# Kernel optimization log

Hardware: AMD Instinct MI355X
Metric: run time of the kernel (lower is better)

## Reference

```python
import jax, jax.numpy as jnp
import numpy as np

# SemiConv2d with semifield_type='MaxMin':
#   out[n,oc,i,j] = max_{ic,kh,kw} min(x_pad[n,ic,i+kh,j+kw], kernel[oc,ic,kh,kw])
# stride=1, 'same' padding with -inf (identity of max).

def setup_inputs() -> dict:
    key = jax.random.key(0)
    kx, kk = jax.random.split(key)
    x = jax.random.normal(kx, (8, 32, 96, 96), dtype=jnp.float32)
    kernel = jax.random.normal(kk, (32, 32, 3, 3), dtype=jnp.float32)
    return {"x": x, "kernel": kernel}


def reference(x, kernel):
    N, IC, H, W = x.shape
    OC, IC2, KH, KW = kernel.shape
    assert IC == IC2
    # same padding for k=3, stride=1 (left=top=1, right=bottom=1)
    p = KH - 1
    top = left = p // 2
    bot = right = p - top
    xp = jnp.pad(x, ((0, 0), (0, 0), (top, bot), (left, right)),
                 constant_values=-jnp.inf)
    out = None
    # small fixed loop over kernel taps (KH*KW = 9); vectorized over N, OC, IC, H, W
    for kh in range(KH):
        for kw in range(KW):
            win = xp[:, :, kh:kh + H, kw:kw + W]           # [N, IC, H, W]
            k_tap = kernel[:, :, kh, kw]                   # [OC, IC]
            # min over values, max over input channels -> [N, OC, H, W]
            v = jnp.max(jnp.minimum(win[:, None], k_tap[None, :, :, None, None]), axis=2)
            out = v if out is None else jnp.maximum(out, v)
    return out
```

## Files before the change

kernel.cpp:

```cpp
#include <hip/hip_runtime.h>
#include <math.h>
#include <stdint.h>


#define HH 96
#define WW 96
#define CIN 32
#define OCN 32
#define XQ_ROWS 98
#define XQ_W 48
#define XQ_SLICE (XQ_ROWS * XQ_W)
#define XQ_TOTAL (256 * XQ_SLICE)
#define NROW 96
#define TBL_BYTES ((size_t)32 * NROW * 16)
#define RMX_BYTES ((size_t)32 * NROW * 4)
#define WS_NEED ((size_t)XQ_TOTAL * 8 + TBL_BYTES + RMX_BYTES)
#define NEGH2 0xFC00FC00u

typedef _Float16 h2 __attribute__((ext_vector_type(2)));
typedef uint32_t u2a4 __attribute__((ext_vector_type(2), aligned(4)));

__device__ __forceinline__ uint32_t pkmin_vs(uint32_t x, uint32_t k) {
    uint32_t d;
    asm("v_pk_min_f16 %0, %1, %2" : "=v"(d) : "v"(x), "s"(k));
    return d;
}
__device__ __forceinline__ uint32_t pkmin_vv(uint32_t a, uint32_t b) {
    uint32_t d;
    asm("v_pk_min_f16 %0, %1, %2" : "=v"(d) : "v"(a), "v"(b));
    return d;
}
__device__ __forceinline__ uint32_t pkmax(uint32_t a, uint32_t b) {
    uint32_t d;
    asm("v_pk_max_f16 %0, %1, %2" : "=v"(d) : "v"(a), "v"(b));
    return d;
}
__device__ __forceinline__ uint32_t packh2(float lo, float hi) {
    h2 p = {(_Float16)lo, (_Float16)hi};
    return __builtin_bit_cast(uint32_t, p);
}

__global__ __launch_bounds__(256) void setup_xq(const float* __restrict__ x,
                                                uint2* __restrict__ xq) {
    int idx = blockIdx.x * 256 + threadIdx.x;
    int j  = idx % XQ_W;
    int t  = idx / XQ_W;
    int hp = t % XQ_ROWS;
    int s  = t / XQ_ROWS;
    int h  = hp - 1;
    bool hv = (h >= 0) && (h < HH);
    const float* row = x + ((size_t)s * HH + (hv ? h : 0)) * WW;
    float a = (hv && j > 0)        ? row[2 * j - 1] : -INFINITY;
    float b = hv                   ? row[2 * j]     : -INFINITY;
    float c = hv                   ? row[2 * j + 1] : -INFINITY;
    float d = (hv && j < XQ_W - 1) ? row[2 * j + 2] : -INFINITY;
    uint2 v;
    v.x = packh2(a, b);
    v.y = packh2(c, d);
    xq[idx] = v;
}

__global__ void setup_row(const float* __restrict__ kk, uint4* __restrict__ tbl,
                          uint32_t* __restrict__ rmx) {
    __shared__ float rs[NROW];
    const int oc = blockIdx.x;
    const int t  = threadIdx.x;
    const int ic = t / 3, dh = t - ic * 3;
    const float* kp = kk + ((size_t)(oc * CIN + ic) * 3 + dh) * 3;
    float k0 = kp[0], k1 = kp[1], k2 = kp[2];
    float rm = fmaxf(fmaxf(k0, k1), k2);
    rs[t] = rm;
    __syncthreads();
    int rank = 0;
    for (int s = 0; s < NROW; ++s) {
        float v = rs[s];
        rank += (v > rm) || (v == rm && s < t);
    }
    uint32_t off = (uint32_t)(ic * XQ_ROWS + dh) * (XQ_W * 8);
    tbl[oc * NROW + rank] = make_uint4(packh2(k0, k0), packh2(k1, k1),
                                       packh2(k2, k2), off);
    rmx[oc * NROW + rank] = packh2(rm, rm);
}

__global__ __launch_bounds__(192, 8) void semiconv_row(const char* __restrict__ xqb,
                                                       const uint4* __restrict__ tbl,
                                                       const uint32_t* __restrict__ rmx,
                                                       float* __restrict__ out) {
    const int tid = threadIdx.x;
    const int jj = tid % 48;
    const int hr = tid / 48;
    const int b  = blockIdx.x;
    const int hp = b % 24;
    const int t  = b / 24;
    const int oc = t & 31;
    const int n  = t >> 5;
    const int h  = hp * 4 + hr;

    const char* xb = xqb + (size_t)n * CIN * XQ_SLICE * 8
                         + (size_t)(h * XQ_W + jj) * 8;
    const uint4* tb = tbl + oc * NROW;
    const uint32_t* rb = rmx + oc * NROW;

    uint32_t acc = NEGH2;
    uint4 e0 = tb[0], e1 = tb[1];

    for (int c = 0; c < NROW / 2; ++c) {
        uint4 f0, f1; uint32_t fr;
        if (c < NROW / 2 - 1) {
            const uint4* nb = tb + 2 * c + 2;
            f0 = nb[0]; f1 = nb[1];
            fr = rb[2 * c + 2];
        }
        u2a4 q0 = *(const u2a4*)(xb + e0.w);
        u2a4 q1 = *(const u2a4*)(xb + e1.w);
        uint32_t v01 = __builtin_amdgcn_alignbit(q0.y, q0.x, 16);
        uint32_t v11 = __builtin_amdgcn_alignbit(q1.y, q1.x, 16);
        uint32_t m0 = pkmax(pkmin_vs(q0.x, e0.x), pkmin_vs(v01, e0.y));
        m0 = pkmax(m0, pkmin_vs(q0.y, e0.z));
        uint32_t m1 = pkmax(pkmin_vs(q1.x, e1.x), pkmin_vs(v11, e1.y));
        m1 = pkmax(m1, pkmin_vs(q1.y, e1.z));
        acc = pkmax(acc, pkmax(m0, m1));

        if (c < NROW / 2 - 1) {
            uint32_t sw = __builtin_amdgcn_alignbit(acc, acc, 16);
            uint32_t mn = pkmin_vv(acc, sw);
            h2 a  = __builtin_bit_cast(h2, mn);
            h2 kn = __builtin_bit_cast(h2, fr);
            if (__all((float)a.x >= (float)kn.x)) break;
            e0 = f0; e1 = f1;
        }
    }

    h2 a = __builtin_bit_cast(h2, acc);
    float2 v = make_float2((float)a.x, (float)a.y);
    *(float2*)(out + (((size_t)(n * OCN + oc)) * HH + h) * WW + 2 * jj) = v;
}

#define NEGINF (-INFINITY)
__global__ __launch_bounds__(192, 8) void semiconv2d_f32(
    const float* __restrict__ x, const float* __restrict__ kk, float* __restrict__ out)
{
    const int tid = threadIdx.x;
    const int w  = tid % WW;
    const int hr = tid / WW;
    const int b   = blockIdx.x;
    const int ocb = b & 7;
    const int hp  = (b >> 3) % 48;
    const int n   = (b >> 3) / 48;
    const int h   = hp * 2 + hr;
    const int oc0 = ocb * 4;
    float a0[4], a1[4], a2[4];
#pragma unroll
    for (int i = 0; i < 4; ++i) { a0[i] = NEGINF; a1[i] = NEGINF; a2[i] = NEGINF; }
    const bool vm = (h > 0), vp = (h < HH - 1);
    const int hm  = vm ? h - 1 : h;
    const int hpl = vp ? h + 1 : h;
    const int cm  = (w > 0) ? -1 : 0;
    const int cp  = (w < WW - 1) ? 1 : 0;
    const float* rm = x + ((size_t)(n * CIN) * HH + hm)  * WW + w;
    const float* r1 = x + ((size_t)(n * CIN) * HH + h)   * WW + w;
    const float* rp = x + ((size_t)(n * CIN) * HH + hpl) * WW + w;
#pragma unroll 2
    for (int ic = 0; ic < CIN; ++ic) {
        float r00 = vm ? rm[cm] : NEGINF, r01 = vm ? rm[0] : NEGINF, r02 = vm ? rm[cp] : NEGINF;
        float r10 = r1[cm], r11 = r1[0], r12 = r1[cp];
        float r20 = vp ? rp[cm] : NEGINF, r21 = vp ? rp[0] : NEGINF, r22 = vp ? rp[cp] : NEGINF;
#pragma unroll
        for (int oc = 0; oc < 4; ++oc) {
            const float* kq = kk + (size_t)(((oc0 + oc) * CIN + ic)) * 9;
            a0[oc] = fmaxf(fmaxf(a0[oc], fminf(r00, kq[0])), fmaxf(fminf(r10, kq[3]), fminf(r20, kq[6])));
            a1[oc] = fmaxf(fmaxf(a1[oc], fminf(r01, kq[1])), fmaxf(fminf(r11, kq[4]), fminf(r21, kq[7])));
            a2[oc] = fmaxf(fmaxf(a2[oc], fminf(r02, kq[2])), fmaxf(fminf(r12, kq[5]), fminf(r22, kq[8])));
        }
        rm += HH * WW; r1 += HH * WW; rp += HH * WW;
    }
#pragma unroll
    for (int oc = 0; oc < 4; ++oc) {
        float v0 = (w > 0)      ? a0[oc] : NEGINF;
        float v2 = (w < WW - 1) ? a2[oc] : NEGINF;
        out[(((size_t)(n * OCN + oc0 + oc)) * HH + h) * WW + w] = fmaxf(fmaxf(v0, a1[oc]), v2);
    }
}

extern "C" void kernel_launch(void* const* d_in, const int* in_sizes, int n_in,
                              void* d_out, int out_size, void* d_ws, size_t ws_size,
                              hipStream_t stream) {
    const float* x  = (const float*)d_in[0];
    const float* kk = (const float*)d_in[1];
    float* out      = (float*)d_out;
    if (ws_size >= WS_NEED) {
        uint2*    xq  = (uint2*)d_ws;
        uint4*    tbl = (uint4*)((char*)d_ws + (size_t)XQ_TOTAL * 8);
        uint32_t* rmx = (uint32_t*)((char*)d_ws + (size_t)XQ_TOTAL * 8 + TBL_BYTES);
        setup_xq<<<dim3(XQ_TOTAL / 256), dim3(256), 0, stream>>>(x, xq);
        setup_row<<<dim3(32), dim3(NROW), 0, stream>>>(kk, tbl, rmx);
        semiconv_row<<<dim3(8 * 32 * 24), dim3(192), 0, stream>>>(
            (const char*)xq, tbl, rmx, out);
    } else {
        semiconv2d_f32<<<dim3(8 * 48 * 8), dim3(192), 0, stream>>>(x, kk, out);
    }
}
```

Measured before the change: 98.71 us.

## Compute four output channels per thread with grouped sorted tap table

The main kernel now has each thread compute four output channels from one load of the packed fp16 input. It walks a per-group table sorted by the group-wide maximum kernel row value, which amortizes input loads and table-entry reads across channels. The two setup kernels are merged into one launch to save a launch. The trade-off is that early exit now needs all four channels to saturate against a looser group bound, so more rows may be processed. Register pressure also rises from holding eight uint4 table entries.

```diff
diff --git a/kernel.cpp b/kernel.cpp
--- a/kernel.cpp
+++ b/kernel.cpp
@@ -11,10 +11,11 @@
 #define XQ_W 48
 #define XQ_SLICE (XQ_ROWS * XQ_W)
 #define XQ_TOTAL (256 * XQ_SLICE)
+#define XQB (XQ_TOTAL / 256)
 #define NROW 96
-#define TBL_BYTES ((size_t)32 * NROW * 16)
-#define RMX_BYTES ((size_t)32 * NROW * 4)
-#define WS_NEED ((size_t)XQ_TOTAL * 8 + TBL_BYTES + RMX_BYTES)
+#define NOCG 8
+#define TBLG_BYTES ((size_t)NOCG * NROW * 64)
+#define WS_NEED ((size_t)XQ_TOTAL * 8 + TBLG_BYTES)
 #define NEGH2 0xFC00FC00u
 
 typedef _Float16 h2 __attribute__((ext_vector_type(2)));
@@ -40,100 +41,138 @@
     return __builtin_bit_cast(uint32_t, p);
 }
 
-__global__ __launch_bounds__(256) void setup_xq(const float* __restrict__ x,
-                                                uint2* __restrict__ xq) {
-    int idx = blockIdx.x * 256 + threadIdx.x;
-    int j  = idx % XQ_W;
-    int t  = idx / XQ_W;
-    int hp = t % XQ_ROWS;
-    int s  = t / XQ_ROWS;
-    int h  = hp - 1;
-    bool hv = (h >= 0) && (h < HH);
-    const float* row = x + ((size_t)s * HH + (hv ? h : 0)) * WW;
-    float a = (hv && j > 0)        ? row[2 * j - 1] : -INFINITY;
-    float b = hv                   ? row[2 * j]     : -INFINITY;
-    float c = hv                   ? row[2 * j + 1] : -INFINITY;
-    float d = (hv && j < XQ_W - 1) ? row[2 * j + 2] : -INFINITY;
-    uint2 v;
-    v.x = packh2(a, b);
-    v.y = packh2(c, d);
-    xq[idx] = v;
-}
-
-__global__ void setup_row(const float* __restrict__ kk, uint4* __restrict__ tbl,
-                          uint32_t* __restrict__ rmx) {
+__global__ __launch_bounds__(256) void setup_all(const float* __restrict__ x,
+                                                 const float* __restrict__ kk,
+                                                 uint2* __restrict__ xq,
+                                                 uint4* __restrict__ tblg) {
     __shared__ float rs[NROW];
-    const int oc = blockIdx.x;
-    const int t  = threadIdx.x;
-    const int ic = t / 3, dh = t - ic * 3;
-    const float* kp = kk + ((size_t)(oc * CIN + ic) * 3 + dh) * 3;
-    float k0 = kp[0], k1 = kp[1], k2 = kp[2];
-    float rm = fmaxf(fmaxf(k0, k1), k2);
-    rs[t] = rm;
+    const int bb = blockIdx.x;
+    if (bb < XQB) {
+        int idx = bb * 256 + threadIdx.x;
+        int j  = idx % XQ_W;
+        int t  = idx / XQ_W;
+        int hp = t % XQ_ROWS;
+        int s  = t / XQ_ROWS;
+        int h  = hp - 1;
+        bool hv = (h >= 0) && (h < HH);
+        const float* row = x + ((size_t)s * HH + (hv ? h : 0)) * WW;
+        float a = (hv && j > 0)        ? row[2 * j - 1] : -INFINITY;
+        float b = hv                   ? row[2 * j]     : -INFINITY;
+        float c = hv                   ? row[2 * j + 1] : -INFINITY;
+        float d = (hv && j < XQ_W - 1) ? row[2 * j + 2] : -INFINITY;
+        uint2 v;
+        v.x = packh2(a, b);
+        v.y = packh2(c, d);
+        xq[idx] = v;
+        return;
+    }
+    const int ocg = bb - XQB;
+    const int t   = threadIdx.x;
+    float kv[12];
+    float gm = -INFINITY;
+    if (t < NROW) {
+        const int ic = t / 3, dh = t - 3 * ic;
+#pragma unroll
+        for (int o = 0; o < 4; ++o) {
+            const float* kp = kk + ((size_t)((ocg * 4 + o) * CIN + ic) * 3 + dh) * 3;
+#pragma unroll
+            for (int w = 0; w < 3; ++w) {
+                float v = kp[w];
+                kv[o * 3 + w] = v;
+                gm = fmaxf(gm, v);
+            }
+        }
+        rs[t] = gm;
+    }
     __syncthreads();
-    int rank = 0;
-    for (int s = 0; s < NROW; ++s) {
-        float v = rs[s];
-        rank += (v > rm) || (v == rm && s < t);
-    }
-    uint32_t off = (uint32_t)(ic * XQ_ROWS + dh) * (XQ_W * 8);
-    tbl[oc * NROW + rank] = make_uint4(packh2(k0, k0), packh2(k1, k1),
-                                       packh2(k2, k2), off);
-    rmx[oc * NROW + rank] = packh2(rm, rm);
-}
-
-__global__ __launch_bounds__(192, 8) void semiconv_row(const char* __restrict__ xqb,
-                                                       const uint4* __restrict__ tbl,
-                                                       const uint32_t* __restrict__ rmx,
-                                                       float* __restrict__ out) {
+    if (t < NROW) {
+        int rank = 0;
+        for (int s = 0; s < NROW; ++s) {
+            float v = rs[s];
+            rank += (v > gm) || (v == gm && s < t);
+        }
+        const int ic = t / 3, dh = t - 3 * ic;
+        uint32_t off = (uint32_t)(ic * XQ_ROWS + dh) * (XQ_W * 8);
+        uint4* e = tblg + ((size_t)ocg * NROW + rank) * 4;
+        e[0] = make_uint4(packh2(kv[0], kv[0]),  packh2(kv[1], kv[1]),
+                          packh2(kv[2], kv[2]),  packh2(kv[3], kv[3]));
+        e[1] = make_uint4(packh2(kv[4], kv[4]),  packh2(kv[5], kv[5]),
+                          packh2(kv[6], kv[6]),  packh2(kv[7], kv[7]));
+        e[2] = make_uint4(packh2(kv[8], kv[8]),  packh2(kv[9], kv[9]),
+                          packh2(kv[10], kv[10]), packh2(kv[11], kv[11]));
+        e[3] = make_uint4(off, packh2(gm, gm), 0u, 0u);
+    }
+}
+
+__global__ __launch_bounds__(192, 8) void semiconv_g4(const char* __restrict__ xqb,
+                                                      const uint4* __restrict__ tblg,
+                                                      float* __restrict__ out) {
     const int tid = threadIdx.x;
     const int jj = tid % 48;
     const int hr = tid / 48;
     const int b  = blockIdx.x;
     const int hp = b % 24;
     const int t  = b / 24;
-    const int oc = t & 31;
-    const int n  = t >> 5;
+    const int ocg = t & 7;
+    const int n   = t >> 3;
     const int h  = hp * 4 + hr;
 
     const char* xb = xqb + (size_t)n * CIN * XQ_SLICE * 8
                          + (size_t)(h * XQ_W + jj) * 8;
-    const uint4* tb = tbl + oc * NROW;
-    const uint32_t* rb = rmx + oc * NROW;
-
-    uint32_t acc = NEGH2;
-    uint4 e0 = tb[0], e1 = tb[1];
+    const uint4* tb = tblg + (size_t)ocg * NROW * 4;
+
+    uint32_t a0 = NEGH2, a1 = NEGH2, a2 = NEGH2, a3 = NEGH2;
+    uint4 eA0 = tb[0], eB0 = tb[1], eC0 = tb[2], eD0 = tb[3];
+    uint4 eA1 = tb[4], eB1 = tb[5], eC1 = tb[6], eD1 = tb[7];
 
     for (int c = 0; c < NROW / 2; ++c) {
-        uint4 f0, f1; uint32_t fr;
+        uint4 fA0, fB0, fC0, fD0, fA1, fB1, fC1, fD1;
         if (c < NROW / 2 - 1) {
-            const uint4* nb = tb + 2 * c + 2;
-            f0 = nb[0]; f1 = nb[1];
-            fr = rb[2 * c + 2];
-        }
-        u2a4 q0 = *(const u2a4*)(xb + e0.w);
-        u2a4 q1 = *(const u2a4*)(xb + e1.w);
+            const uint4* nb = tb + 8 * (c + 1);
+            fA0 = nb[0]; fB0 = nb[1]; fC0 = nb[2]; fD0 = nb[3];
+            fA1 = nb[4]; fB1 = nb[5]; fC1 = nb[6]; fD1 = nb[7];
+        }
+        u2a4 q0 = *(const u2a4*)(xb + eD0.x);
+        u2a4 q1 = *(const u2a4*)(xb + eD1.x);
         uint32_t v01 = __builtin_amdgcn_alignbit(q0.y, q0.x, 16);
         uint32_t v11 = __builtin_amdgcn_alignbit(q1.y, q1.x, 16);
-        uint32_t m0 = pkmax(pkmin_vs(q0.x, e0.x), pkmin_vs(v01, e0.y));
-        m0 = pkmax(m0, pkmin_vs(q0.y, e0.z));
-        uint32_t m1 = pkmax(pkmin_vs(q1.x, e1.x), pkmin_vs(v11, e1.y));
-        m1 = pkmax(m1, pkmin_vs(q1.y, e1.z));
-        acc = pkmax(acc, pkmax(m0, m1));
+        a0 = pkmax(a0, pkmax(pkmax(pkmin_vs(q0.x, eA0.x), pkmin_vs(v01, eA0.y)),
+                             pkmin_vs(q0.y, eA0.z)));
+        a1 = pkmax(a1, pkmax(pkmax(pkmin_vs(q0.x, eA0.w), pkmin_vs(v01, eB0.x)),
+                             pkmin_vs(q0.y, eB0.y)));
+        a2 = pkmax(a2, pkmax(pkmax(pkmin_vs(q0.x, eB0.z), pkmin_vs(v01, eB0.w)),
+                             pkmin_vs(q0.y, eC0.x)));
+        a3 = pkmax(a3, pkmax(pkmax(pkmin_vs(q0.x, eC0.y), pkmin_vs(v01, eC0.z)),
+                             pkmin_vs(q0.y, eC0.w)));
+        a0 = pkmax(a0, pkmax(pkmax(pkmin_vs(q1.x, eA1.x), pkmin_vs(v11, eA1.y)),
+                             pkmin_vs(q1.y, eA1.z)));
+        a1 = pkmax(a1, pkmax(pkmax(pkmin_vs(q1.x, eA1.w), pkmin_vs(v11, eB1.x)),
+                             pkmin_vs(q1.y, eB1.y)));
+        a2 = pkmax(a2, pkmax(pkmax(pkmin_vs(q1.x, eB1.z), pkmin_vs(v11, eB1.w)),
+                             pkmin_vs(q1.y, eC1.x)));
+        a3 = pkmax(a3, pkmax(pkmax(pkmin_vs(q1.x, eC1.y), pkmin_vs(v11, eC1.z)),
+                             pkmin_vs(q1.y, eC1.w)));
 
         if (c < NROW / 2 - 1) {
-            uint32_t sw = __builtin_amdgcn_alignbit(acc, acc, 16);
-            uint32_t mn = pkmin_vv(acc, sw);
-            h2 a  = __builtin_bit_cast(h2, mn);
-            h2 kn = __builtin_bit_cast(h2, fr);
-            if (__all((float)a.x >= (float)kn.x)) break;
-            e0 = f0; e1 = f1;
-        }
-    }
-
-    h2 a = __builtin_bit_cast(h2, acc);
-    float2 v = make_float2((float)a.x, (float)a.y);
-    *(float2*)(out + (((size_t)(n * OCN + oc)) * HH + h) * WW + 2 * jj) = v;
+            uint32_t mn = pkmin_vv(pkmin_vv(a0, a1), pkmin_vv(a2, a3));
+            mn = pkmin_vv(mn, __builtin_amdgcn_alignbit(mn, mn, 16));
+            h2 aa = __builtin_bit_cast(h2, mn);
+            h2 kn = __builtin_bit_cast(h2, fD0.y);
+            if (__all((float)aa.x >= (float)kn.x)) break;
+            eA0 = fA0; eB0 = fB0; eC0 = fC0; eD0 = fD0;
+            eA1 = fA1; eB1 = fB1; eC1 = fC1; eD1 = fD1;
+        }
+    }
+
+    float* ob = out + (((size_t)(n * OCN + ocg * 4)) * HH + h) * WW + 2 * jj;
+    h2 r0 = __builtin_bit_cast(h2, a0);
+    h2 r1 = __builtin_bit_cast(h2, a1);
+    h2 r2 = __builtin_bit_cast(h2, a2);
+    h2 r3 = __builtin_bit_cast(h2, a3);
+    *(float2*)(ob)                  = make_float2((float)r0.x, (float)r0.y);
+    *(float2*)(ob + HH * WW)        = make_float2((float)r1.x, (float)r1.y);
+    *(float2*)(ob + 2 * HH * WW)    = make_float2((float)r2.x, (float)r2.y);
+    *(float2*)(ob + 3 * HH * WW)    = make_float2((float)r3.x, (float)r3.y);
 }
 
 #define NEGINF (-INFINITY)
@@ -189,13 +228,11 @@
     const float* kk = (const float*)d_in[1];
     float* out      = (float*)d_out;
     if (ws_size >= WS_NEED) {
-        uint2*    xq  = (uint2*)d_ws;
-        uint4*    tbl = (uint4*)((char*)d_ws + (size_t)XQ_TOTAL * 8);
-        uint32_t* rmx = (uint32_t*)((char*)d_ws + (size_t)XQ_TOTAL * 8 + TBL_BYTES);
-        setup_xq<<<dim3(XQ_TOTAL / 256), dim3(256), 0, stream>>>(x, xq);
-        setup_row<<<dim3(32), dim3(NROW), 0, stream>>>(kk, tbl, rmx);
-        semiconv_row<<<dim3(8 * 32 * 24), dim3(192), 0, stream>>>(
-            (const char*)xq, tbl, rmx, out);
+        uint2* xq   = (uint2*)d_ws;
+        uint4* tblg = (uint4*)((char*)d_ws + (size_t)XQ_TOTAL * 8);
+        setup_all<<<dim3(XQB + NOCG), dim3(256), 0, stream>>>(x, kk, xq, tblg);
+        semiconv_g4<<<dim3(8 * NOCG * 24), dim3(192), 0, stream>>>(
+            (const char*)xq, tblg, out);
     } else {
         semiconv2d_f32<<<dim3(8 * 48 * 8), dim3(192), 0, stream>>>(x, kk, out);
     }
```

Result: slower. 105.7 us (+7.1%).

## Compact fp16 input layout, fuse setup kernels, process four kernel rows per step

Applied to the files above, without the earlier changes.

The padded fp16 input copy now stores each row as a dense 200-byte run of halves with 4-byte-aligned overlapping reads, replacing the previous duplicated 8-bytes-per-pair layout. This roughly halves the workspace write and read traffic. The two setup kernels are merged into one launch, removing a launch and a dependency. The main loop now handles four sorted kernel rows per iteration instead of two and drops the software prefetch, which gives more loads in flight but checks for early exit less often and may do extra work.

```diff
diff --git a/kernel.cpp b/kernel.cpp
--- a/kernel.cpp
+++ b/kernel.cpp
@@ -8,13 +8,16 @@
 #define CIN 32
 #define OCN 32
 #define XQ_ROWS 98
-#define XQ_W 48
-#define XQ_SLICE (XQ_ROWS * XQ_W)
-#define XQ_TOTAL (256 * XQ_SLICE)
+#define ROWB 200
+#define SLICEB (XQ_ROWS * ROWB)
+#define XQ_BYTES ((size_t)256 * SLICEB)
+#define ROWU2 25
+#define XQW_TOTAL (256 * XQ_ROWS * ROWU2)
+#define XQWB (XQW_TOTAL / 256)
 #define NROW 96
-#define TBL_BYTES ((size_t)32 * NROW * 16)
-#define RMX_BYTES ((size_t)32 * NROW * 4)
-#define WS_NEED ((size_t)XQ_TOTAL * 8 + TBL_BYTES + RMX_BYTES)
+#define TBL_BYTES ((size_t)OCN * NROW * 16)
+#define RMX_BYTES ((size_t)OCN * NROW * 4)
+#define WS_NEED (XQ_BYTES + TBL_BYTES + RMX_BYTES)
 #define NEGH2 0xFC00FC00u
 
 typedef _Float16 h2 __attribute__((ext_vector_type(2)));
@@ -40,32 +43,38 @@
     return __builtin_bit_cast(uint32_t, p);
 }
 
-__global__ __launch_bounds__(256) void setup_xq(const float* __restrict__ x,
-                                                uint2* __restrict__ xq) {
-    int idx = blockIdx.x * 256 + threadIdx.x;
-    int j  = idx % XQ_W;
-    int t  = idx / XQ_W;
-    int hp = t % XQ_ROWS;
-    int s  = t / XQ_ROWS;
-    int h  = hp - 1;
-    bool hv = (h >= 0) && (h < HH);
-    const float* row = x + ((size_t)s * HH + (hv ? h : 0)) * WW;
-    float a = (hv && j > 0)        ? row[2 * j - 1] : -INFINITY;
-    float b = hv                   ? row[2 * j]     : -INFINITY;
-    float c = hv                   ? row[2 * j + 1] : -INFINITY;
-    float d = (hv && j < XQ_W - 1) ? row[2 * j + 2] : -INFINITY;
-    uint2 v;
-    v.x = packh2(a, b);
-    v.y = packh2(c, d);
-    xq[idx] = v;
-}
-
-__global__ void setup_row(const float* __restrict__ kk, uint4* __restrict__ tbl,
-                          uint32_t* __restrict__ rmx) {
+__global__ __launch_bounds__(256) void setup_all(const float* __restrict__ x,
+                                                 const float* __restrict__ kk,
+                                                 uint2* __restrict__ xq,
+                                                 uint4* __restrict__ tbl,
+                                                 uint32_t* __restrict__ rmx) {
     __shared__ float rs[NROW];
-    const int oc = blockIdx.x;
+    const int bb = blockIdx.x;
+    if (bb < XQWB) {
+        int idx = bb * 256 + threadIdx.x;
+        int j8 = idx % ROWU2;
+        int t  = idx / ROWU2;
+        int hp = t % XQ_ROWS;
+        int s  = t / XQ_ROWS;
+        int h  = hp - 1;
+        bool hv = (h >= 0) && (h < HH);
+        const float* row = x + ((size_t)s * HH + (hv ? h : 0)) * WW;
+        float v[4];
+#pragma unroll
+        for (int q = 0; q < 4; ++q) {
+            int w = 4 * j8 - 1 + q;
+            v[q] = (hv && w >= 0 && w < WW) ? row[w] : -INFINITY;
+        }
+        uint2 o;
+        o.x = packh2(v[0], v[1]);
+        o.y = packh2(v[2], v[3]);
+        xq[idx] = o;
+        return;
+    }
+    const int oc = bb - XQWB;
     const int t  = threadIdx.x;
-    const int ic = t / 3, dh = t - ic * 3;
+    if (t >= NROW) return;
+    const int ic = t / 3, dh = t - 3 * ic;
     const float* kp = kk + ((size_t)(oc * CIN + ic) * 3 + dh) * 3;
     float k0 = kp[0], k1 = kp[1], k2 = kp[2];
     float rm = fmaxf(fmaxf(k0, k1), k2);
@@ -76,16 +85,16 @@
         float v = rs[s];
         rank += (v > rm) || (v == rm && s < t);
     }
-    uint32_t off = (uint32_t)(ic * XQ_ROWS + dh) * (XQ_W * 8);
+    uint32_t off = (uint32_t)(ic * XQ_ROWS + dh) * ROWB;
     tbl[oc * NROW + rank] = make_uint4(packh2(k0, k0), packh2(k1, k1),
                                        packh2(k2, k2), off);
     rmx[oc * NROW + rank] = packh2(rm, rm);
 }
 
-__global__ __launch_bounds__(192, 8) void semiconv_row(const char* __restrict__ xqb,
-                                                       const uint4* __restrict__ tbl,
-                                                       const uint32_t* __restrict__ rmx,
-                                                       float* __restrict__ out) {
+__global__ __launch_bounds__(192, 8) void semiconv_c(const char* __restrict__ xqb,
+                                                     const uint4* __restrict__ tbl,
+                                                     const uint32_t* __restrict__ rmx,
+                                                     float* __restrict__ out) {
     const int tid = threadIdx.x;
     const int jj = tid % 48;
     const int hr = tid / 48;
@@ -96,38 +105,45 @@
     const int n  = t >> 5;
     const int h  = hp * 4 + hr;
 
-    const char* xb = xqb + (size_t)n * CIN * XQ_SLICE * 8
-                         + (size_t)(h * XQ_W + jj) * 8;
+    const char* xqn = xqb + (size_t)n * CIN * SLICEB;
+    const int vbyte = h * ROWB + 4 * jj;
     const uint4* tb = tbl + oc * NROW;
     const uint32_t* rb = rmx + oc * NROW;
 
     uint32_t acc = NEGH2;
-    uint4 e0 = tb[0], e1 = tb[1];
-
-    for (int c = 0; c < NROW / 2; ++c) {
-        uint4 f0, f1; uint32_t fr;
-        if (c < NROW / 2 - 1) {
-            const uint4* nb = tb + 2 * c + 2;
-            f0 = nb[0]; f1 = nb[1];
-            fr = rb[2 * c + 2];
-        }
-        u2a4 q0 = *(const u2a4*)(xb + e0.w);
-        u2a4 q1 = *(const u2a4*)(xb + e1.w);
-        uint32_t v01 = __builtin_amdgcn_alignbit(q0.y, q0.x, 16);
-        uint32_t v11 = __builtin_amdgcn_alignbit(q1.y, q1.x, 16);
-        uint32_t m0 = pkmax(pkmin_vs(q0.x, e0.x), pkmin_vs(v01, e0.y));
-        m0 = pkmax(m0, pkmin_vs(q0.y, e0.z));
-        uint32_t m1 = pkmax(pkmin_vs(q1.x, e1.x), pkmin_vs(v11, e1.y));
-        m1 = pkmax(m1, pkmin_vs(q1.y, e1.z));
-        acc = pkmax(acc, pkmax(m0, m1));
-
-        if (c < NROW / 2 - 1) {
+
+    for (int c = 0; c < NROW / 4; ++c) {
+        uint4 e0 = tb[4 * c], e1 = tb[4 * c + 1], e2 = tb[4 * c + 2], e3 = tb[4 * c + 3];
+        uint32_t kn = (c < NROW / 4 - 1) ? rb[4 * c + 4] : 0u;
+
+        const char* r0 = xqn + e0.w;
+        const char* r1 = xqn + e1.w;
+        const char* r2 = xqn + e2.w;
+        const char* r3 = xqn + e3.w;
+        u2a4 q0 = *(const u2a4*)(r0 + vbyte);
+        u2a4 q1 = *(const u2a4*)(r1 + vbyte);
+        u2a4 q2 = *(const u2a4*)(r2 + vbyte);
+        u2a4 q3 = *(const u2a4*)(r3 + vbyte);
+        uint32_t v0 = __builtin_amdgcn_alignbit(q0.y, q0.x, 16);
+        uint32_t v1 = __builtin_amdgcn_alignbit(q1.y, q1.x, 16);
+        uint32_t v2 = __builtin_amdgcn_alignbit(q2.y, q2.x, 16);
+        uint32_t v3 = __builtin_amdgcn_alignbit(q3.y, q3.x, 16);
+        uint32_t m0 = pkmax(pkmax(pkmin_vs(q0.x, e0.x), pkmin_vs(v0, e0.y)),
+                            pkmin_vs(q0.y, e0.z));
+        uint32_t m1 = pkmax(pkmax(pkmin_vs(q1.x, e1.x), pkmin_vs(v1, e1.y)),
+                            pkmin_vs(q1.y, e1.z));
+        uint32_t m2 = pkmax(pkmax(pkmin_vs(q2.x, e2.x), pkmin_vs(v2, e2.y)),
+                            pkmin_vs(q2.y, e2.z));
+        uint32_t m3 = pkmax(pkmax(pkmin_vs(q3.x, e3.x), pkmin_vs(v3, e3.y)),
+                            pkmin_vs(q3.y, e3.z));
+        acc = pkmax(acc, pkmax(pkmax(m0, m1), pkmax(m2, m3)));
+
+        if (c < NROW / 4 - 1) {
             uint32_t sw = __builtin_amdgcn_alignbit(acc, acc, 16);
             uint32_t mn = pkmin_vv(acc, sw);
             h2 a  = __builtin_bit_cast(h2, mn);
-            h2 kn = __builtin_bit_cast(h2, fr);
-            if (__all((float)a.x >= (float)kn.x)) break;
-            e0 = f0; e1 = f1;
+            h2 kv = __builtin_bit_cast(h2, kn);
+            if (__all((float)a.x >= (float)kv.x)) break;
         }
     }
 
@@ -190,11 +206,10 @@
     float* out      = (float*)d_out;
     if (ws_size >= WS_NEED) {
         uint2*    xq  = (uint2*)d_ws;
-        uint4*    tbl = (uint4*)((char*)d_ws + (size_t)XQ_TOTAL * 8);
-        uint32_t* rmx = (uint32_t*)((char*)d_ws + (size_t)XQ_TOTAL * 8 + TBL_BYTES);
-        setup_xq<<<dim3(XQ_TOTAL / 256), dim3(256), 0, stream>>>(x, xq);
-        setup_row<<<dim3(32), dim3(NROW), 0, stream>>>(kk, tbl, rmx);
-        semiconv_row<<<dim3(8 * 32 * 24), dim3(192), 0, stream>>>(
+        uint4*    tbl = (uint4*)((char*)d_ws + XQ_BYTES);
+        uint32_t* rmx = (uint32_t*)((char*)d_ws + XQ_BYTES + TBL_BYTES);
+        setup_all<<<dim3(XQWB + OCN), dim3(256), 0, stream>>>(x, kk, xq, tbl, rmx);
+        semiconv_c<<<dim3(8 * OCN * 24), dim3(192), 0, stream>>>(
             (const char*)xq, tbl, rmx, out);
     } else {
         semiconv2d_f32<<<dim3(8 * 48 * 8), dim3(192), 0, stream>>>(x, kk, out);
```

Result: faster. 89.29 us (-9.5%).
